# Kernel tuning notes

Measured on AMD Instinct MI355X. Metric: run time of the kernel, lower is better.

## Reference

```python
import jax, jax.numpy as jnp
import numpy as np

B, F, D, E = 16384, 2048, 256, 8  # batch, feature, expert out dim, n instrument experts (+1 default)


def setup_inputs() -> dict:
    key = jax.random.key(0)
    k1, k2, k3 = jax.random.split(key, 3)
    shared_features = jax.random.normal(k1, (B, F), dtype=jnp.float32)
    # instrument ids 0..E-1; id_to_index is the identity mapping here
    instrument_ids = jax.random.randint(k2, (B, 1), 0, E, dtype=jnp.int32)
    # stacked expert weights: E instrument layers + 1 default layer => E+1 Dense(F->D)
    W = jax.random.normal(k3, (E + 1, F, D), dtype=jnp.float32) * 0.02
    b = jnp.zeros((E + 1, D), dtype=jnp.float32)
    return {"shared_features": shared_features, "W": W, "b": b,
            "instrument_ids": instrument_ids}


def reference(shared_features, W, b, instrument_ids):
    # Compute ALL expert projections on the full batch (faithful to the TF layer),
    # stacked on axis=1: [B, E+1, D]
    stacked = jnp.einsum('bf,efd->bed', shared_features, W) + b
    # id_to_index lookup: ids are 0..E-1, identity mapping; default layer at index E unused
    idx = instrument_ids[:, 0].astype(jnp.int32)  # [B]
    # gather_nd equivalent: select per-sample expert output -> [B, D]
    selected = jnp.take_along_axis(stacked, idx[:, None, None], axis=1)[:, 0, :]
    return selected
```

## Files before the change

kernel.cpp:

```cpp
#include <hip/hip_runtime.h>
#include <hip/hip_bf16.h>

#define B_SZ 16384
#define F_SZ 2048
#define D_SZ 256
#define E_SZ 8
#define GRID_G 528

typedef __attribute__((ext_vector_type(8))) short bhalf8;
typedef __attribute__((ext_vector_type(4))) float fl4;

__device__ __forceinline__ short f2b(float f) {
  __hip_bfloat16 h = __float2bfloat16(f);
  union { __hip_bfloat16 h; short s; } u;
  u.h = h;
  return u.s;
}

__global__ void k_scatter(const int* __restrict__ ids, int* __restrict__ counts,
                          int* __restrict__ perm) {
  __shared__ int lcnt[E_SZ], lbase[E_SZ];
  int t = threadIdx.x;
  if (t < E_SZ) lcnt[t] = 0;
  __syncthreads();
  int b = blockIdx.x * 256 + t;
  int e = ids[b];
  int p = atomicAdd(&lcnt[e], 1);
  __syncthreads();
  if (t < E_SZ) lbase[t] = atomicAdd(&counts[t], lcnt[t]);
  __syncthreads();
  perm[e * B_SZ + lbase[e] + p] = b;
}

__global__ void k_transpose(const float* __restrict__ W, __hip_bfloat16* __restrict__ Wt) {
  __shared__ float tile[64][65];
  int e = blockIdx.z;
  int f0 = blockIdx.x * 64;
  int d0 = blockIdx.y * 64;
  int t = threadIdx.x;
  const float* src = W + ((size_t)e * F_SZ + f0) * D_SZ + d0;
  int fr = t >> 2, c0 = t & 3;
#pragma unroll
  for (int c = c0; c < 16; c += 4) {
    float4 v = *(const float4*)(src + (size_t)fr * D_SZ + c * 4);
    tile[fr][c * 4 + 0] = v.x;
    tile[fr][c * 4 + 1] = v.y;
    tile[fr][c * 4 + 2] = v.z;
    tile[fr][c * 4 + 3] = v.w;
  }
  __syncthreads();
  int dr = t >> 2, cc = t & 3;
  union { unsigned short u[16]; bhalf8 v[2]; } pk;
#pragma unroll
  for (int k = 0; k < 16; ++k) pk.u[k] = (unsigned short)f2b(tile[cc * 16 + k][dr]);
  __hip_bfloat16* dst = Wt + ((size_t)e * D_SZ + d0 + dr) * F_SZ + f0 + cc * 16;
  ((bhalf8*)dst)[0] = pk.v[0];
  ((bhalf8*)dst)[1] = pk.v[1];
}

__device__ __forceinline__ void load_lds16(const __hip_bfloat16* g, __hip_bfloat16* l) {
  __builtin_amdgcn_global_load_lds((const __attribute__((address_space(1))) void*)g,
                                   (__attribute__((address_space(3))) void*)l, 16, 0, 0);
}

__launch_bounds__(256, 2)
__global__ void k_gemm(const float* __restrict__ x, const __hip_bfloat16* __restrict__ Wt,
                       const float* __restrict__ bias, const int* __restrict__ counts,
                       const int* __restrict__ perm, float* __restrict__ out) {
  int id = blockIdx.x;
  int nb = (id & 1) * 128;
  int mt = id >> 1;
  int e = -1, mbase = 0, count = 0;
  {
    int acc = 0;
#pragma unroll
    for (int ee = 0; ee < E_SZ; ++ee) {
      int c = counts[ee];
      int nt = (c + 63) >> 6;
      if (e < 0 && mt < acc + nt) { e = ee; mbase = (mt - acc) * 64; count = c; }
      acc += nt;
    }
  }
  if (e < 0) return;

  __shared__ __align__(16) __hip_bfloat16 As[64 * 64];
  __shared__ __align__(16) __hip_bfloat16 Bs[128 * 64];

  int t = threadIdx.x;
  int w = t >> 6;
  int lane = t & 63;
  int wm = w >> 1, wn = w & 1;
  int l15 = lane & 15;
  int q = lane >> 4;

  const int* permE = perm + e * B_SZ;

  int tr = t >> 4;
  int tc = t & 15;
  const float* pA[4];
  int wAo[4];
#pragma unroll
  for (int i = 0; i < 4; ++i) {
    int r = i * 16 + tr;
    int gm = mbase + r;
    int src = permE[(gm < count) ? gm : mbase];
    pA[i] = x + (size_t)src * F_SZ + tc * 4;
    int cw = tc >> 1, half = tc & 1;
    wAo[i] = r * 64 + ((cw ^ (r & 7)) * 8) + half * 4;
  }

  const __hip_bfloat16* pB[4];
  __hip_bfloat16* dstB[4];
#pragma unroll
  for (int i = 0; i < 4; ++i) {
    int c = i * 256 + t;
    int n = c >> 3;
    int cl = (c & 7) ^ (n & 7);
    pB[i] = Wt + (size_t)(e * D_SZ + nb + n) * F_SZ + cl * 8;
    dstB[i] = Bs + (size_t)(i * 256 + w * 64) * 8;
  }

  int rAo[2][2], rBo[2][4];
#pragma unroll
  for (int ks = 0; ks < 2; ++ks) {
#pragma unroll
    for (int i = 0; i < 2; ++i) {
      int m = wm * 32 + i * 16 + l15;
      rAo[ks][i] = m * 64 + (((ks * 4 + q) ^ (m & 7)) * 8);
    }
#pragma unroll
    for (int j = 0; j < 4; ++j) {
      int n = wn * 64 + j * 16 + l15;
      rBo[ks][j] = n * 64 + (((ks * 4 + q) ^ (n & 7)) * 8);
    }
  }

  fl4 zz = {0.0f, 0.0f, 0.0f, 0.0f};
  fl4 acc[2][4];
#pragma unroll
  for (int i = 0; i < 2; ++i)
#pragma unroll
    for (int j = 0; j < 4; ++j) acc[i][j] = zz;

  for (int k0 = 0; k0 < F_SZ; k0 += 64) {
    __syncthreads();

    float4 av[4];
#pragma unroll
    for (int i = 0; i < 4; ++i) av[i] = *(const float4*)(pA[i] + k0);
#pragma unroll
    for (int i = 0; i < 4; ++i) load_lds16(pB[i] + k0, dstB[i]);
#pragma unroll
    for (int i = 0; i < 4; ++i) {
      short4 s;
      s.x = f2b(av[i].x); s.y = f2b(av[i].y);
      s.z = f2b(av[i].z); s.w = f2b(av[i].w);
      *(short4*)(As + wAo[i]) = s;
    }

    __syncthreads();

#pragma unroll
    for (int ks = 0; ks < 2; ++ks) {
      bhalf8 af[2], bf[4];
#pragma unroll
      for (int i = 0; i < 2; ++i) af[i] = *(const bhalf8*)(As + rAo[ks][i]);
#pragma unroll
      for (int j = 0; j < 4; ++j) bf[j] = *(const bhalf8*)(Bs + rBo[ks][j]);
#pragma unroll
      for (int i = 0; i < 2; ++i)
#pragma unroll
        for (int j = 0; j < 4; ++j)
          acc[i][j] = __builtin_amdgcn_mfma_f32_16x16x32_bf16(af[i], bf[j], acc[i][j], 0, 0, 0);
    }
  }

  float bv[4];
#pragma unroll
  for (int j = 0; j < 4; ++j) bv[j] = bias[e * D_SZ + nb + wn * 64 + j * 16 + l15];

#pragma unroll
  for (int i = 0; i < 2; ++i) {
#pragma unroll
    for (int r = 0; r < 4; ++r) {
      int gm = mbase + wm * 32 + i * 16 + q * 4 + r;
      if (gm < count) {
        int row = permE[gm];
        float* po = out + (size_t)row * D_SZ + nb + wn * 64;
#pragma unroll
        for (int j = 0; j < 4; ++j) po[j * 16 + l15] = acc[i][j][r] + bv[j];
      }
    }
  }
}

extern "C" void kernel_launch(void* const* d_in, const int* in_sizes, int n_in,
                              void* d_out, int out_size, void* d_ws, size_t ws_size,
                              hipStream_t stream) {
  const float* x = (const float*)d_in[0];
  const float* W = (const float*)d_in[1];
  const float* bias = (const float*)d_in[2];
  const int* ids = (const int*)d_in[3];
  float* out = (float*)d_out;

  char* ws = (char*)d_ws;
  int* counts = (int*)ws;
  int* perm = (int*)(ws + 256);
  __hip_bfloat16* Wt = (__hip_bfloat16*)(ws + (1 << 20));

  hipMemsetAsync(counts, 0, E_SZ * sizeof(int), stream);
  k_scatter<<<B_SZ / 256, 256, 0, stream>>>(ids, counts, perm);
  k_transpose<<<dim3(F_SZ / 64, D_SZ / 64, E_SZ), 256, 0, stream>>>(W, Wt);
  k_gemm<<<GRID_G, 256, 0, stream>>>(x, Wt, bias, counts, perm, out);
}
```

Before: 259.2 us.

## Double-buffer LDS tiles and widen GEMM blocks to 512 threads with prefetch

```diff
diff --git a/kernel.cpp b/kernel.cpp
--- a/kernel.cpp
+++ b/kernel.cpp
@@ -63,7 +63,7 @@
                                    (__attribute__((address_space(3))) void*)l, 16, 0, 0);
 }
 
-__launch_bounds__(256, 2)
+__launch_bounds__(512, 4)
 __global__ void k_gemm(const float* __restrict__ x, const __hip_bfloat16* __restrict__ Wt,
                        const float* __restrict__ bias, const int* __restrict__ counts,
                        const int* __restrict__ perm, float* __restrict__ out) {
@@ -72,24 +72,24 @@
   int mt = id >> 1;
   int e = -1, mbase = 0, count = 0;
   {
-    int acc = 0;
+    int acc0 = 0;
 #pragma unroll
     for (int ee = 0; ee < E_SZ; ++ee) {
       int c = counts[ee];
       int nt = (c + 63) >> 6;
-      if (e < 0 && mt < acc + nt) { e = ee; mbase = (mt - acc) * 64; count = c; }
-      acc += nt;
+      if (e < 0 && mt < acc0 + nt) { e = ee; mbase = (mt - acc0) * 64; count = c; }
+      acc0 += nt;
     }
   }
   if (e < 0) return;
 
-  __shared__ __align__(16) __hip_bfloat16 As[64 * 64];
-  __shared__ __align__(16) __hip_bfloat16 Bs[128 * 64];
+  __shared__ __align__(16) __hip_bfloat16 As[2 * 64 * 64];
+  __shared__ __align__(16) __hip_bfloat16 Bs[2 * 128 * 64];
 
   int t = threadIdx.x;
   int w = t >> 6;
   int lane = t & 63;
-  int wm = w >> 1, wn = w & 1;
+  int wm = w >> 2, wn = w & 3;
   int l15 = lane & 15;
   int q = lane >> 4;
 
@@ -97,11 +97,11 @@
 
   int tr = t >> 4;
   int tc = t & 15;
-  const float* pA[4];
-  int wAo[4];
-#pragma unroll
-  for (int i = 0; i < 4; ++i) {
-    int r = i * 16 + tr;
+  const float* pA[2];
+  int wAo[2];
+#pragma unroll
+  for (int i = 0; i < 2; ++i) {
+    int r = i * 32 + tr;
     int gm = mbase + r;
     int src = permE[(gm < count) ? gm : mbase];
     pA[i] = x + (size_t)src * F_SZ + tc * 4;
@@ -109,18 +109,18 @@
     wAo[i] = r * 64 + ((cw ^ (r & 7)) * 8) + half * 4;
   }
 
-  const __hip_bfloat16* pB[4];
-  __hip_bfloat16* dstB[4];
-#pragma unroll
-  for (int i = 0; i < 4; ++i) {
-    int c = i * 256 + t;
-    int n = c >> 3;
-    int cl = (c & 7) ^ (n & 7);
+  const __hip_bfloat16* pB[2];
+  int dB[2];
+#pragma unroll
+  for (int i = 0; i < 2; ++i) {
+    int p = i * 512 + t;
+    int n = p >> 3;
+    int cl = (p & 7) ^ (n & 7);
     pB[i] = Wt + (size_t)(e * D_SZ + nb + n) * F_SZ + cl * 8;
-    dstB[i] = Bs + (size_t)(i * 256 + w * 64) * 8;
-  }
-
-  int rAo[2][2], rBo[2][4];
+    dB[i] = i * 4096 + w * 512;
+  }
+
+  int rAo[2][2], rBo[2][2];
 #pragma unroll
   for (int ks = 0; ks < 2; ++ks) {
 #pragma unroll
@@ -129,55 +129,103 @@
       rAo[ks][i] = m * 64 + (((ks * 4 + q) ^ (m & 7)) * 8);
     }
 #pragma unroll
-    for (int j = 0; j < 4; ++j) {
-      int n = wn * 64 + j * 16 + l15;
+    for (int j = 0; j < 2; ++j) {
+      int n = wn * 32 + j * 16 + l15;
       rBo[ks][j] = n * 64 + (((ks * 4 + q) ^ (n & 7)) * 8);
     }
   }
 
   fl4 zz = {0.0f, 0.0f, 0.0f, 0.0f};
-  fl4 acc[2][4];
+  fl4 acc[2][2];
 #pragma unroll
   for (int i = 0; i < 2; ++i)
 #pragma unroll
-    for (int j = 0; j < 4; ++j) acc[i][j] = zz;
-
-  for (int k0 = 0; k0 < F_SZ; k0 += 64) {
-    __syncthreads();
-
-    float4 av[4];
-#pragma unroll
-    for (int i = 0; i < 4; ++i) av[i] = *(const float4*)(pA[i] + k0);
-#pragma unroll
-    for (int i = 0; i < 4; ++i) load_lds16(pB[i] + k0, dstB[i]);
-#pragma unroll
-    for (int i = 0; i < 4; ++i) {
+    for (int j = 0; j < 2; ++j) acc[i][j] = zz;
+
+  float4 av[2];
+
+#pragma unroll
+  for (int i = 0; i < 2; ++i) load_lds16(pB[i], Bs + dB[i]);
+  __builtin_amdgcn_sched_barrier(0);
+#pragma unroll
+  for (int i = 0; i < 2; ++i) av[i] = *(const float4*)(pA[i]);
+#pragma unroll
+  for (int i = 0; i < 2; ++i) {
+    short4 s;
+    s.x = f2b(av[i].x); s.y = f2b(av[i].y);
+    s.z = f2b(av[i].z); s.w = f2b(av[i].w);
+    *(short4*)(As + wAo[i]) = s;
+  }
+#pragma unroll
+  for (int i = 0; i < 2; ++i) av[i] = *(const float4*)(pA[i] + 64);
+  __builtin_amdgcn_sched_barrier(0);
+  asm volatile("s_waitcnt vmcnt(2) lgkmcnt(0)");
+  __builtin_amdgcn_sched_barrier(0);
+  __builtin_amdgcn_s_barrier();
+  __builtin_amdgcn_sched_barrier(0);
+
+  for (int k = 0; k < 31; ++k) {
+    int cb = (k & 1);
+    int nx = cb ^ 1;
+#pragma unroll
+    for (int i = 0; i < 2; ++i) load_lds16(pB[i] + (k + 1) * 64, Bs + nx * 8192 + dB[i]);
+    __builtin_amdgcn_sched_barrier(0);
+#pragma unroll
+    for (int i = 0; i < 2; ++i) {
       short4 s;
       s.x = f2b(av[i].x); s.y = f2b(av[i].y);
       s.z = f2b(av[i].z); s.w = f2b(av[i].w);
-      *(short4*)(As + wAo[i]) = s;
-    }
-
-    __syncthreads();
-
+      *(short4*)(As + nx * 4096 + wAo[i]) = s;
+    }
+    int kn = (k + 2) & 31;
+#pragma unroll
+    for (int i = 0; i < 2; ++i) av[i] = *(const float4*)(pA[i] + kn * 64);
+    {
+      const __hip_bfloat16* Ab = As + cb * 4096;
+      const __hip_bfloat16* Bb = Bs + cb * 8192;
+#pragma unroll
+      for (int ks = 0; ks < 2; ++ks) {
+        bhalf8 af[2], bf[2];
+#pragma unroll
+        for (int i = 0; i < 2; ++i) af[i] = *(const bhalf8*)(Ab + rAo[ks][i]);
+#pragma unroll
+        for (int j = 0; j < 2; ++j) bf[j] = *(const bhalf8*)(Bb + rBo[ks][j]);
+#pragma unroll
+        for (int i = 0; i < 2; ++i)
+#pragma unroll
+          for (int j = 0; j < 2; ++j)
+            acc[i][j] = __builtin_amdgcn_mfma_f32_16x16x32_bf16(af[i], bf[j], acc[i][j], 0, 0, 0);
+      }
+    }
+    __builtin_amdgcn_sched_barrier(0);
+    asm volatile("s_waitcnt vmcnt(2) lgkmcnt(0)");
+    __builtin_amdgcn_sched_barrier(0);
+    __builtin_amdgcn_s_barrier();
+    __builtin_amdgcn_sched_barrier(0);
+  }
+  asm volatile("" :: "v"(av[0].x), "v"(av[1].x));
+
+  {
+    const __hip_bfloat16* Ab = As + 4096;
+    const __hip_bfloat16* Bb = Bs + 8192;
 #pragma unroll
     for (int ks = 0; ks < 2; ++ks) {
-      bhalf8 af[2], bf[4];
-#pragma unroll
-      for (int i = 0; i < 2; ++i) af[i] = *(const bhalf8*)(As + rAo[ks][i]);
-#pragma unroll
-      for (int j = 0; j < 4; ++j) bf[j] = *(const bhalf8*)(Bs + rBo[ks][j]);
+      bhalf8 af[2], bf[2];
+#pragma unroll
+      for (int i = 0; i < 2; ++i) af[i] = *(const bhalf8*)(Ab + rAo[ks][i]);
+#pragma unroll
+      for (int j = 0; j < 2; ++j) bf[j] = *(const bhalf8*)(Bb + rBo[ks][j]);
 #pragma unroll
       for (int i = 0; i < 2; ++i)
 #pragma unroll
-        for (int j = 0; j < 4; ++j)
+        for (int j = 0; j < 2; ++j)
           acc[i][j] = __builtin_amdgcn_mfma_f32_16x16x32_bf16(af[i], bf[j], acc[i][j], 0, 0, 0);
     }
   }
 
-  float bv[4];
-#pragma unroll
-  for (int j = 0; j < 4; ++j) bv[j] = bias[e * D_SZ + nb + wn * 64 + j * 16 + l15];
+  float bv[2];
+#pragma unroll
+  for (int j = 0; j < 2; ++j) bv[j] = bias[e * D_SZ + nb + wn * 32 + j * 16 + l15];
 
 #pragma unroll
   for (int i = 0; i < 2; ++i) {
@@ -186,9 +234,9 @@
       int gm = mbase + wm * 32 + i * 16 + q * 4 + r;
       if (gm < count) {
         int row = permE[gm];
-        float* po = out + (size_t)row * D_SZ + nb + wn * 64;
-#pragma unroll
-        for (int j = 0; j < 4; ++j) po[j * 16 + l15] = acc[i][j][r] + bv[j];
+        float* po = out + (size_t)row * D_SZ + nb + wn * 32;
+#pragma unroll
+        for (int j = 0; j < 2; ++j) po[j * 16 + l15] = acc[i][j][r] + bv[j];
       }
     }
   }
@@ -211,5 +259,5 @@
   hipMemsetAsync(counts, 0, E_SZ * sizeof(int), stream);
   k_scatter<<<B_SZ / 256, 256, 0, stream>>>(ids, counts, perm);
   k_transpose<<<dim3(F_SZ / 64, D_SZ / 64, E_SZ), 256, 0, stream>>>(W, Wt);
-  k_gemm<<<GRID_G, 256, 0, stream>>>(x, Wt, bias, counts, perm, out);
-}
+  k_gemm<<<GRID_G, 512, 0, stream>>>(x, Wt, bias, counts, perm, out);
+}
```

Result: faster. 253.0 us (-2.4%).
